# Optimization experiments

Hardware: AMD Instinct MI355X
Metric: run time of the kernel (lower is better)

Reference implementation:

```python
import jax, jax.numpy as jnp
import numpy as np

B, C, N, K = 2, 64, 20000, 16
COUT = 64


def setup_inputs() -> dict:
    key = jax.random.key(0)
    k1, k2, k3, k4, k5 = jax.random.split(key, 5)
    x = jax.random.normal(k1, (B, C, N, 1), dtype=jnp.float32)
    edge_index = jax.random.randint(k2, (2, B, N, K), 0, N)
    pos = jax.random.normal(k3, (B, 3, N, 1), dtype=jnp.float32)
    # BasicConv([2C, COUT]) -> 1x1 Conv2d weight [COUT, 2C] (+bias), then ReLU
    W = jax.random.normal(k4, (COUT, 2 * C), dtype=jnp.float32) * (1.0 / np.sqrt(2 * C))
    b = jax.random.normal(k5, (COUT,), dtype=jnp.float32) * 0.01
    return {"x": x, "edge_index": edge_index, "pos": pos, "W": W, "b": b}


def _gather(t, idx):
    # t: [B, C, N, 1], idx: [B, N, K] -> [B, C, N, K]
    t3 = t[..., 0]  # [B, C, N]
    return jax.vmap(lambda tb, ib: tb[:, ib])(t3, idx)


def reference(x, edge_index, pos, W, b):
    x_i = _gather(x, edge_index[1])           # [B, C, N, K] center
    x_j = _gather(x, edge_index[0])           # [B, C, N, K] neighbor
    feat = jnp.concatenate([x_i, x_j - x_i], axis=1)  # [B, 2C, N, K]
    # 1x1 conv + bias + ReLU
    out = jnp.einsum('oc,bcnk->bonk', W, feat) + b[None, :, None, None]
    out = jax.nn.relu(out)
    # distance-based suppression
    pos_i = _gather(pos, edge_index[1])       # [B, 3, N, K]
    pos_j = _gather(pos, edge_index[0])
    dis = jnp.sqrt(jnp.sum(jnp.square(pos_j - pos_i), axis=1))  # [B, N, K]
    suppression = 2.0 * jax.nn.sigmoid(-dis)[:, None, :, :]     # [B, 1, N, K]
    out = out * suppression
    max_value = jnp.max(out, axis=-1, keepdims=True)             # [B, COUT, N, 1]
    return max_value
```

## Files before the change

### kernel.cpp

```cpp
#include <hip/hip_runtime.h>
#include <math.h>

#define B_    2
#define C_    64
#define N_    20000
#define K_    16
#define COUT_ 64
#define TN1   64
#define NB1   ((N_ + TN1 - 1) / TN1)
#define TN2   16
#define NB2   (N_ / TN2)

typedef unsigned int   u32;
typedef unsigned short u16;

static __device__ __forceinline__ u16 f2bf(float f) {
    union { float f; u32 u; } v; v.f = f;
    u32 r = (v.u + 0x7FFFu + ((v.u >> 16) & 1u)) >> 16;
    return (u16)r;
}
static __device__ __forceinline__ float uasf(u32 u) {
    union { u32 u; float f; } v; v.u = u; return v.f;
}

__global__ __launch_bounds__(256)
void stage1(const float* __restrict__ x, const float* __restrict__ W,
            const float* __restrict__ bias,
            u16* __restrict__ zbuf, u16* __restrict__ ybuf) {
    __shared__ float xt[64][68];
    __shared__ float wc[64][130];

    const int bi   = blockIdx.x;
    const int b    = bi / NB1;
    const int n0   = (bi % NB1) * TN1;
    const int t    = threadIdx.x;
    const int lane = t & 63;
    const int w    = t >> 6;

    #pragma unroll
    for (int r = 0; r < 16; ++r) {
        int flat = r * 256 + t;
        int o = flat >> 6, c = flat & 63;
        float w1 = W[o * 128 + c];
        float w2 = W[o * 128 + 64 + c];
        wc[c][2 * o]     = w1 - w2;
        wc[c][2 * o + 1] = w2;
    }
    const float* xb = x + (size_t)b * C_ * N_;
    #pragma unroll
    for (int r = 0; r < 4; ++r) {
        int flat = r * 256 + t;
        int c = flat >> 4, ng = (flat & 15) * 4;
        int n = n0 + ng;
        float4 v;
        if (n + 3 < N_) {
            v = *(const float4*)&xb[c * N_ + n];
        } else {
            v.x = (n     < N_) ? xb[c * N_ + n    ] : 0.0f;
            v.y = (n + 1 < N_) ? xb[c * N_ + n + 1] : 0.0f;
            v.z = (n + 2 < N_) ? xb[c * N_ + n + 2] : 0.0f;
            v.w = (n + 3 < N_) ? xb[c * N_ + n + 3] : 0.0f;
        }
        *(float4*)&xt[c][ng] = v;
    }
    const float bo = bias[lane];
    __syncthreads();

    const int nb = w * 16;
    float4 z0 = {bo,bo,bo,bo}, z1 = z0, z2 = z0, z3 = z0;
    float4 y0 = {0,0,0,0},     y1 = y0, y2 = y0, y3 = y0;

#define FMA4(ZR, YR, XV) \
    ZR.x = fmaf(wv.x, XV.x, ZR.x);  YR.x = fmaf(wv.y, XV.x, YR.x); \
    ZR.y = fmaf(wv.x, XV.y, ZR.y);  YR.y = fmaf(wv.y, XV.y, YR.y); \
    ZR.z = fmaf(wv.x, XV.z, ZR.z);  YR.z = fmaf(wv.y, XV.z, YR.z); \
    ZR.w = fmaf(wv.x, XV.w, ZR.w);  YR.w = fmaf(wv.y, XV.w, YR.w);

    #pragma unroll 2
    for (int c = 0; c < 64; ++c) {
        float2 wv = *(const float2*)&wc[c][2 * lane];
        float4 xa = *(const float4*)&xt[c][nb];
        float4 xv1 = *(const float4*)&xt[c][nb + 4];
        float4 xv2 = *(const float4*)&xt[c][nb + 8];
        float4 xv3 = *(const float4*)&xt[c][nb + 12];
        FMA4(z0, y0, xa)
        FMA4(z1, y1, xv1)
        FMA4(z2, y2, xv2)
        FMA4(z3, y3, xv3)
    }
#undef FMA4

    {
        const size_t rowb = (size_t)b * N_;
        auto st = [&](int i, float zv, float yv) {
            int n = n0 + nb + i;
            if (n < N_) {
                size_t off = (rowb + n) * 64 + lane;
                zbuf[off] = f2bf(zv);
                ybuf[off] = f2bf(yv);
            }
        };
        st(0,  z0.x, y0.x); st(1,  z0.y, y0.y); st(2,  z0.z, y0.z); st(3,  z0.w, y0.w);
        st(4,  z1.x, y1.x); st(5,  z1.y, y1.y); st(6,  z1.z, y1.z); st(7,  z1.w, y1.w);
        st(8,  z2.x, y2.x); st(9,  z2.y, y2.y); st(10, z2.z, y2.z); st(11, z2.w, y2.w);
        st(12, z3.x, y3.x); st(13, z3.y, y3.y); st(14, z3.z, y3.z); st(15, z3.w, y3.w);
    }
}

__global__ __launch_bounds__(256)
void stage2(const int* __restrict__ ei, const float* __restrict__ pos,
            const u16* __restrict__ zbuf, const u16* __restrict__ ybuf,
            float* __restrict__ out) {
    __shared__ uint2 esl[TN2][17];
    __shared__ float tile[TN2][66];

    const int bi   = blockIdx.x;
    const int b    = bi / NB2;
    const int n0   = (bi % NB2) * TN2;
    const int t    = threadIdx.x;
    const int nl   = t >> 4;
    const int kh   = (t >> 3) & 1;
    const int cq   = t & 7;

    {
        const int    idx = n0 * K_ + t;
        const int*   e0  = ei + (size_t)b * N_ * K_;
        const int*   e1  = ei + ((size_t)B_ + b) * N_ * K_;
        const float* pb  = pos + (size_t)b * 3 * N_;
        int i0 = e0[idx], i1 = e1[idx];
        float dx = pb[i0]          - pb[i1];
        float dy = pb[N_ + i0]     - pb[N_ + i1];
        float dz = pb[2 * N_ + i0] - pb[2 * N_ + i1];
        float dis = sqrtf(dx * dx + dy * dy + dz * dz);
        float s = 2.0f / (1.0f + __expf(dis));
        esl[t >> 4][t & 15] = make_uint2((u32)i0 | ((u32)i1 << 16),
                                         __float_as_uint(s));
    }
    __syncthreads();

    const u16* zb = zbuf + (size_t)b * N_ * 64;
    const u16* yb = ybuf + (size_t)b * N_ * 64;

    float4 ma = {0,0,0,0}, mb = {0,0,0,0};

#define COMB(ZW, YW, MLO, MHI) { \
    float zl = uasf((ZW) << 16), zh = uasf((ZW) & 0xFFFF0000u); \
    float yl = uasf((YW) << 16), yh = uasf((YW) & 0xFFFF0000u); \
    MLO = fmaxf(MLO, fmaxf(zl + yl, 0.0f) * s); \
    MHI = fmaxf(MHI, fmaxf(zh + yh, 0.0f) * s); }

    #pragma unroll
    for (int i = 0; i < 8; ++i) {
        int   k = 2 * i + kh;
        uint2 e = esl[nl][k];
        int   i0 = (int)(e.x & 0xFFFFu);
        int   i1 = (int)(e.x >> 16);
        float s  = uasf(e.y);
        uint4 z4 = *((const uint4*)(zb + ((size_t)i1 << 6)) + cq);
        uint4 y4 = *((const uint4*)(yb + ((size_t)i0 << 6)) + cq);
        COMB(z4.x, y4.x, ma.x, ma.y)
        COMB(z4.y, y4.y, ma.z, ma.w)
        COMB(z4.z, y4.z, mb.x, mb.y)
        COMB(z4.w, y4.w, mb.z, mb.w)
    }
#undef COMB

    ma.x = fmaxf(ma.x, __shfl_xor(ma.x, 8));
    ma.y = fmaxf(ma.y, __shfl_xor(ma.y, 8));
    ma.z = fmaxf(ma.z, __shfl_xor(ma.z, 8));
    ma.w = fmaxf(ma.w, __shfl_xor(ma.w, 8));
    mb.x = fmaxf(mb.x, __shfl_xor(mb.x, 8));
    mb.y = fmaxf(mb.y, __shfl_xor(mb.y, 8));
    mb.z = fmaxf(mb.z, __shfl_xor(mb.z, 8));
    mb.w = fmaxf(mb.w, __shfl_xor(mb.w, 8));

    if (kh == 0) {
        int cb = cq * 8;
        *(float2*)&tile[nl][cb]     = make_float2(ma.x, ma.y);
        *(float2*)&tile[nl][cb + 2] = make_float2(ma.z, ma.w);
        *(float2*)&tile[nl][cb + 4] = make_float2(mb.x, mb.y);
        *(float2*)&tile[nl][cb + 6] = make_float2(mb.z, mb.w);
    }
    __syncthreads();

    #pragma unroll
    for (int r = 0; r < 4; ++r) {
        int flat = r * 256 + t;
        int o = flat >> 4, n2 = flat & 15;
        __builtin_nontemporal_store(tile[n2][o],
            &out[((size_t)b * COUT_ + o) * N_ + n0 + n2]);
    }
}

extern "C" void kernel_launch(void* const* d_in, const int* in_sizes, int n_in,
                              void* d_out, int out_size, void* d_ws, size_t ws_size,
                              hipStream_t stream) {
    const float* x    = (const float*)d_in[0];
    const int*   ei   = (const int*)  d_in[1];
    const float* pos  = (const float*)d_in[2];
    const float* W    = (const float*)d_in[3];
    const float* bias = (const float*)d_in[4];
    float*       out  = (float*)d_out;

    const size_t tabElems = (size_t)B_ * N_ * 64;
    u16* zbuf = (u16*)d_ws;
    u16* ybuf = zbuf + tabElems;

    hipLaunchKernelGGL(stage1, dim3(B_ * NB1), dim3(256), 0, stream,
                       x, W, bias, zbuf, ybuf);
    hipLaunchKernelGGL(stage2, dim3(B_ * NB2), dim3(256), 0, stream,
                       ei, pos, zbuf, ybuf, out);
}
```

Baseline: 107.9 us.

## Split gather tables into channel halves and precompute edge data in separate kernel

Stage1 now writes the z/y bf16 tables split into two 32-channel halves, and stage2 runs one block per channel half, so each block gathers from a half-sized table region that may fit better in cache. Edge indices and distance suppression factors are computed once in a new edgeprep kernel and stored as packed uint2, which removes the redundant per-block pos gathers. Stage2 reads these from global memory and reduces across four k-slices with two shuffle rounds. The trade-off is an extra kernel launch plus a round trip of the edge buffer through memory, and the edge data is now read twice, once per channel half.

```diff
diff --git a/kernel.cpp b/kernel.cpp
--- a/kernel.cpp
+++ b/kernel.cpp
@@ -10,6 +10,7 @@
 #define NB1   ((N_ + TN1 - 1) / TN1)
 #define TN2   16
 #define NB2   (N_ / TN2)
+#define NCH   2
 
 typedef unsigned int   u32;
 typedef unsigned short u16;
@@ -21,6 +22,22 @@
 }
 static __device__ __forceinline__ float uasf(u32 u) {
     union { u32 u; float f; } v; v.u = u; return v.f;
+}
+
+__global__ __launch_bounds__(256)
+void edgeprep(const int* __restrict__ ei, const float* __restrict__ pos,
+              uint2* __restrict__ ebuf) {
+    const int g  = blockIdx.x * 256 + threadIdx.x;
+    const int b  = g / (N_ * K_);
+    const int i0 = ei[g];
+    const int i1 = ei[B_ * N_ * K_ + g];
+    const float* pb = pos + (size_t)b * 3 * N_;
+    float dx = pb[i0]          - pb[i1];
+    float dy = pb[N_ + i0]     - pb[N_ + i1];
+    float dz = pb[2 * N_ + i0] - pb[2 * N_ + i1];
+    float dis = sqrtf(dx * dx + dy * dy + dz * dz);
+    float s = 2.0f / (1.0f + __expf(dis));
+    ebuf[g] = make_uint2((u32)i0 | ((u32)i1 << 16), __float_as_uint(s));
 }
 
 __global__ __launch_bounds__(256)
@@ -91,11 +108,11 @@
 #undef FMA4
 
     {
-        const size_t rowb = (size_t)b * N_;
+        const size_t chb = ((size_t)(lane >> 5) * B_ + b) * N_;
         auto st = [&](int i, float zv, float yv) {
             int n = n0 + nb + i;
             if (n < N_) {
-                size_t off = (rowb + n) * 64 + lane;
+                size_t off = (chb + n) * 32 + (lane & 31);
                 zbuf[off] = f2bf(zv);
                 ybuf[off] = f2bf(yv);
             }
@@ -108,38 +125,24 @@
 }
 
 __global__ __launch_bounds__(256)
-void stage2(const int* __restrict__ ei, const float* __restrict__ pos,
+void stage2(const uint2* __restrict__ ebuf,
             const u16* __restrict__ zbuf, const u16* __restrict__ ybuf,
             float* __restrict__ out) {
-    __shared__ uint2 esl[TN2][17];
-    __shared__ float tile[TN2][66];
-
-    const int bi   = blockIdx.x;
-    const int b    = bi / NB2;
-    const int n0   = (bi % NB2) * TN2;
-    const int t    = threadIdx.x;
-    const int nl   = t >> 4;
-    const int kh   = (t >> 3) & 1;
-    const int cq   = t & 7;
-
-    {
-        const int    idx = n0 * K_ + t;
-        const int*   e0  = ei + (size_t)b * N_ * K_;
-        const int*   e1  = ei + ((size_t)B_ + b) * N_ * K_;
-        const float* pb  = pos + (size_t)b * 3 * N_;
-        int i0 = e0[idx], i1 = e1[idx];
-        float dx = pb[i0]          - pb[i1];
-        float dy = pb[N_ + i0]     - pb[N_ + i1];
-        float dz = pb[2 * N_ + i0] - pb[2 * N_ + i1];
-        float dis = sqrtf(dx * dx + dy * dy + dz * dz);
-        float s = 2.0f / (1.0f + __expf(dis));
-        esl[t >> 4][t & 15] = make_uint2((u32)i0 | ((u32)i1 << 16),
-                                         __float_as_uint(s));
-    }
-    __syncthreads();
-
-    const u16* zb = zbuf + (size_t)b * N_ * 64;
-    const u16* yb = ybuf + (size_t)b * N_ * 64;
+    __shared__ float tile[TN2][34];
+
+    const int bi  = blockIdx.x;
+    const int b   = bi / (NCH * NB2);
+    const int rem = bi % (NCH * NB2);
+    const int ch  = rem / NB2;
+    const int n0  = (rem % NB2) * TN2;
+    const int t   = threadIdx.x;
+    const int nl  = t >> 4;
+    const int ks  = (t >> 2) & 3;
+    const int cq  = t & 3;
+
+    const uint2* eb = ebuf + (size_t)b * N_ * K_ + (size_t)(n0 + nl) * K_ + ks;
+    const u16*   zb = zbuf + ((size_t)ch * B_ + b) * N_ * 32;
+    const u16*   yb = ybuf + ((size_t)ch * B_ + b) * N_ * 32;
 
     float4 ma = {0,0,0,0}, mb = {0,0,0,0};
 
@@ -150,14 +153,13 @@
     MHI = fmaxf(MHI, fmaxf(zh + yh, 0.0f) * s); }
 
     #pragma unroll
-    for (int i = 0; i < 8; ++i) {
-        int   k = 2 * i + kh;
-        uint2 e = esl[nl][k];
+    for (int i = 0; i < 4; ++i) {
+        uint2 e = eb[4 * i];
         int   i0 = (int)(e.x & 0xFFFFu);
         int   i1 = (int)(e.x >> 16);
         float s  = uasf(e.y);
-        uint4 z4 = *((const uint4*)(zb + ((size_t)i1 << 6)) + cq);
-        uint4 y4 = *((const uint4*)(yb + ((size_t)i0 << 6)) + cq);
+        uint4 z4 = *((const uint4*)(zb + ((size_t)i1 << 5)) + cq);
+        uint4 y4 = *((const uint4*)(yb + ((size_t)i0 << 5)) + cq);
         COMB(z4.x, y4.x, ma.x, ma.y)
         COMB(z4.y, y4.y, ma.z, ma.w)
         COMB(z4.z, y4.z, mb.x, mb.y)
@@ -165,6 +167,14 @@
     }
 #undef COMB
 
+    ma.x = fmaxf(ma.x, __shfl_xor(ma.x, 4));
+    ma.y = fmaxf(ma.y, __shfl_xor(ma.y, 4));
+    ma.z = fmaxf(ma.z, __shfl_xor(ma.z, 4));
+    ma.w = fmaxf(ma.w, __shfl_xor(ma.w, 4));
+    mb.x = fmaxf(mb.x, __shfl_xor(mb.x, 4));
+    mb.y = fmaxf(mb.y, __shfl_xor(mb.y, 4));
+    mb.z = fmaxf(mb.z, __shfl_xor(mb.z, 4));
+    mb.w = fmaxf(mb.w, __shfl_xor(mb.w, 4));
     ma.x = fmaxf(ma.x, __shfl_xor(ma.x, 8));
     ma.y = fmaxf(ma.y, __shfl_xor(ma.y, 8));
     ma.z = fmaxf(ma.z, __shfl_xor(ma.z, 8));
@@ -174,7 +184,7 @@
     mb.z = fmaxf(mb.z, __shfl_xor(mb.z, 8));
     mb.w = fmaxf(mb.w, __shfl_xor(mb.w, 8));
 
-    if (kh == 0) {
+    if (ks == 0) {
         int cb = cq * 8;
         *(float2*)&tile[nl][cb]     = make_float2(ma.x, ma.y);
         *(float2*)&tile[nl][cb + 2] = make_float2(ma.z, ma.w);
@@ -184,11 +194,11 @@
     __syncthreads();
 
     #pragma unroll
-    for (int r = 0; r < 4; ++r) {
+    for (int r = 0; r < 2; ++r) {
         int flat = r * 256 + t;
         int o = flat >> 4, n2 = flat & 15;
         __builtin_nontemporal_store(tile[n2][o],
-            &out[((size_t)b * COUT_ + o) * N_ + n0 + n2]);
+            &out[((size_t)b * COUT_ + ch * 32 + o) * N_ + n0 + n2]);
     }
 }
 
@@ -202,12 +212,15 @@
     const float* bias = (const float*)d_in[4];
     float*       out  = (float*)d_out;
 
-    const size_t tabElems = (size_t)B_ * N_ * 64;
-    u16* zbuf = (u16*)d_ws;
-    u16* ybuf = zbuf + tabElems;
-
+    const size_t tabElems = (size_t)NCH * B_ * N_ * 32;
+    u16*   zbuf = (u16*)d_ws;
+    u16*   ybuf = zbuf + tabElems;
+    uint2* ebuf = (uint2*)(ybuf + tabElems);
+
+    hipLaunchKernelGGL(edgeprep, dim3((B_ * N_ * K_) / 256), dim3(256), 0, stream,
+                       ei, pos, ebuf);
     hipLaunchKernelGGL(stage1, dim3(B_ * NB1), dim3(256), 0, stream,
                        x, W, bias, zbuf, ybuf);
-    hipLaunchKernelGGL(stage2, dim3(B_ * NB2), dim3(256), 0, stream,
-                       ei, pos, zbuf, ybuf, out);
-}
+    hipLaunchKernelGGL(stage2, dim3(B_ * NCH * NB2), dim3(256), 0, stream,
+                       ebuf, zbuf, ybuf, out);
+}
```

Result: slower. 116.9 us (+8.4%).

## Split gather tables into two channel halves and swizzle stage2 block order

Applied to the files above, without the earlier changes.

Stage1 now writes the bf16 z/y tables as two channel-half planes of 32 channels each instead of one 64-channel row per point. Stage2 launches twice as many blocks, each handling one channel half. A block-index swizzle interleaves batch and half so that concurrently scheduled blocks work on different planes, which is meant to shrink the per-block gather working set and improve cache locality of the random row gathers. In exchange, the edge indices and the distance/suppression computation are recomputed for each half, extra shuffle reductions are added, and the edge-index loads become nontemporal.

```diff
diff --git a/kernel.cpp b/kernel.cpp
--- a/kernel.cpp
+++ b/kernel.cpp
@@ -10,6 +10,7 @@
 #define NB1   ((N_ + TN1 - 1) / TN1)
 #define TN2   16
 #define NB2   (N_ / TN2)
+#define NCH   2
 
 typedef unsigned int   u32;
 typedef unsigned short u16;
@@ -91,11 +92,11 @@
 #undef FMA4
 
     {
-        const size_t rowb = (size_t)b * N_;
+        const size_t chb = ((size_t)(lane >> 5) * B_ + b) * N_;
         auto st = [&](int i, float zv, float yv) {
             int n = n0 + nb + i;
             if (n < N_) {
-                size_t off = (rowb + n) * 64 + lane;
+                size_t off = (chb + n) * 32 + (lane & 31);
                 zbuf[off] = f2bf(zv);
                 ybuf[off] = f2bf(yv);
             }
@@ -112,22 +113,27 @@
             const u16* __restrict__ zbuf, const u16* __restrict__ ybuf,
             float* __restrict__ out) {
     __shared__ uint2 esl[TN2][17];
-    __shared__ float tile[TN2][66];
-
-    const int bi   = blockIdx.x;
-    const int b    = bi / NB2;
-    const int n0   = (bi % NB2) * TN2;
+    __shared__ float tile[TN2][34];
+
+    const int bid  = blockIdx.x;
+    const int x8   = bid & 7;
+    const int p    = x8 & 3;
+    const int b    = p >> 1;
+    const int ch   = p & 1;
+    const int tl   = (bid >> 3) * 2 + (x8 >> 2);
+    const int n0   = tl * TN2;
     const int t    = threadIdx.x;
     const int nl   = t >> 4;
-    const int kh   = (t >> 3) & 1;
-    const int cq   = t & 7;
+    const int ks   = (t >> 2) & 3;
+    const int cq   = t & 3;
 
     {
         const int    idx = n0 * K_ + t;
         const int*   e0  = ei + (size_t)b * N_ * K_;
         const int*   e1  = ei + ((size_t)B_ + b) * N_ * K_;
         const float* pb  = pos + (size_t)b * 3 * N_;
-        int i0 = e0[idx], i1 = e1[idx];
+        int i0 = __builtin_nontemporal_load(&e0[idx]);
+        int i1 = __builtin_nontemporal_load(&e1[idx]);
         float dx = pb[i0]          - pb[i1];
         float dy = pb[N_ + i0]     - pb[N_ + i1];
         float dz = pb[2 * N_ + i0] - pb[2 * N_ + i1];
@@ -138,8 +144,8 @@
     }
     __syncthreads();
 
-    const u16* zb = zbuf + (size_t)b * N_ * 64;
-    const u16* yb = ybuf + (size_t)b * N_ * 64;
+    const u16* zb = zbuf + ((size_t)ch * B_ + b) * N_ * 32;
+    const u16* yb = ybuf + ((size_t)ch * B_ + b) * N_ * 32;
 
     float4 ma = {0,0,0,0}, mb = {0,0,0,0};
 
@@ -150,14 +156,13 @@
     MHI = fmaxf(MHI, fmaxf(zh + yh, 0.0f) * s); }
 
     #pragma unroll
-    for (int i = 0; i < 8; ++i) {
-        int   k = 2 * i + kh;
-        uint2 e = esl[nl][k];
+    for (int i = 0; i < 4; ++i) {
+        uint2 e = esl[nl][4 * i + ks];
         int   i0 = (int)(e.x & 0xFFFFu);
         int   i1 = (int)(e.x >> 16);
         float s  = uasf(e.y);
-        uint4 z4 = *((const uint4*)(zb + ((size_t)i1 << 6)) + cq);
-        uint4 y4 = *((const uint4*)(yb + ((size_t)i0 << 6)) + cq);
+        uint4 z4 = *((const uint4*)(zb + ((size_t)i1 << 5)) + cq);
+        uint4 y4 = *((const uint4*)(yb + ((size_t)i0 << 5)) + cq);
         COMB(z4.x, y4.x, ma.x, ma.y)
         COMB(z4.y, y4.y, ma.z, ma.w)
         COMB(z4.z, y4.z, mb.x, mb.y)
@@ -165,6 +170,14 @@
     }
 #undef COMB
 
+    ma.x = fmaxf(ma.x, __shfl_xor(ma.x, 4));
+    ma.y = fmaxf(ma.y, __shfl_xor(ma.y, 4));
+    ma.z = fmaxf(ma.z, __shfl_xor(ma.z, 4));
+    ma.w = fmaxf(ma.w, __shfl_xor(ma.w, 4));
+    mb.x = fmaxf(mb.x, __shfl_xor(mb.x, 4));
+    mb.y = fmaxf(mb.y, __shfl_xor(mb.y, 4));
+    mb.z = fmaxf(mb.z, __shfl_xor(mb.z, 4));
+    mb.w = fmaxf(mb.w, __shfl_xor(mb.w, 4));
     ma.x = fmaxf(ma.x, __shfl_xor(ma.x, 8));
     ma.y = fmaxf(ma.y, __shfl_xor(ma.y, 8));
     ma.z = fmaxf(ma.z, __shfl_xor(ma.z, 8));
@@ -174,7 +187,7 @@
     mb.z = fmaxf(mb.z, __shfl_xor(mb.z, 8));
     mb.w = fmaxf(mb.w, __shfl_xor(mb.w, 8));
 
-    if (kh == 0) {
+    if (ks == 0) {
         int cb = cq * 8;
         *(float2*)&tile[nl][cb]     = make_float2(ma.x, ma.y);
         *(float2*)&tile[nl][cb + 2] = make_float2(ma.z, ma.w);
@@ -184,11 +197,11 @@
     __syncthreads();
 
     #pragma unroll
-    for (int r = 0; r < 4; ++r) {
+    for (int r = 0; r < 2; ++r) {
         int flat = r * 256 + t;
         int o = flat >> 4, n2 = flat & 15;
         __builtin_nontemporal_store(tile[n2][o],
-            &out[((size_t)b * COUT_ + o) * N_ + n0 + n2]);
+            &out[((size_t)b * COUT_ + ch * 32 + o) * N_ + n0 + n2]);
     }
 }
 
@@ -202,12 +215,12 @@
     const float* bias = (const float*)d_in[4];
     float*       out  = (float*)d_out;
 
-    const size_t tabElems = (size_t)B_ * N_ * 64;
+    const size_t tabElems = (size_t)NCH * B_ * N_ * 32;
     u16* zbuf = (u16*)d_ws;
     u16* ybuf = zbuf + tabElems;
 
     hipLaunchKernelGGL(stage1, dim3(B_ * NB1), dim3(256), 0, stream,
                        x, W, bias, zbuf, ybuf);
-    hipLaunchKernelGGL(stage2, dim3(B_ * NB2), dim3(256), 0, stream,
+    hipLaunchKernelGGL(stage2, dim3(B_ * NCH * NB2), dim3(256), 0, stream,
                        ei, pos, zbuf, ybuf, out);
 }
```

Measured after the change: 127.9 us. 18.6% more time.

## Give each stage2 thread a full neighbor loop and double nodes per block

Applied to the files above, without the earlier changes.

The gather-max kernel now assigns one node per 8-thread group, and each thread loops over all 16 neighbors. This replaces the previous split of neighbors across two thread halves followed by a cross-lane shuffle reduction. The tile size grows to 32 nodes per block, and edge-index and distance setup now processes two edges per thread with vectorized int2 loads. The goal is more independent gathers in flight per thread and less reduction overhead, at the cost of half as many blocks and longer per-thread dependency chains. The shared tile row stride changed to 65 while float2 stores remain, so those LDS writes can be misaligned on odd rows.

```diff
diff --git a/kernel.cpp b/kernel.cpp
--- a/kernel.cpp
+++ b/kernel.cpp
@@ -8,7 +8,7 @@
 #define COUT_ 64
 #define TN1   64
 #define NB1   ((N_ + TN1 - 1) / TN1)
-#define TN2   16
+#define TN2   32
 #define NB2   (N_ / TN2)
 
 typedef unsigned int   u32;
@@ -112,34 +112,43 @@
             const u16* __restrict__ zbuf, const u16* __restrict__ ybuf,
             float* __restrict__ out) {
     __shared__ uint2 esl[TN2][17];
-    __shared__ float tile[TN2][66];
-
-    const int bi   = blockIdx.x;
-    const int b    = bi / NB2;
-    const int n0   = (bi % NB2) * TN2;
-    const int t    = threadIdx.x;
-    const int nl   = t >> 4;
-    const int kh   = (t >> 3) & 1;
-    const int cq   = t & 7;
+    __shared__ float tile[TN2][65];
+
+    const int bi  = blockIdx.x;
+    const int b   = bi / NB2;
+    const int n0  = (bi % NB2) * TN2;
+    const int t   = threadIdx.x;
+    const int nl  = t >> 3;
+    const int cq  = t & 7;
 
     {
-        const int    idx = n0 * K_ + t;
+        const int    e2  = 2 * t;
+        const int    idx = n0 * K_ + e2;
         const int*   e0  = ei + (size_t)b * N_ * K_;
         const int*   e1  = ei + ((size_t)B_ + b) * N_ * K_;
         const float* pb  = pos + (size_t)b * 3 * N_;
-        int i0 = e0[idx], i1 = e1[idx];
-        float dx = pb[i0]          - pb[i1];
-        float dy = pb[N_ + i0]     - pb[N_ + i1];
-        float dz = pb[2 * N_ + i0] - pb[2 * N_ + i1];
-        float dis = sqrtf(dx * dx + dy * dy + dz * dz);
-        float s = 2.0f / (1.0f + __expf(dis));
-        esl[t >> 4][t & 15] = make_uint2((u32)i0 | ((u32)i1 << 16),
-                                         __float_as_uint(s));
+        int2 i0p = *(const int2*)&e0[idx];
+        int2 i1p = *(const int2*)&e1[idx];
+        float dx0 = pb[i0p.x]          - pb[i1p.x];
+        float dy0 = pb[N_ + i0p.x]     - pb[N_ + i1p.x];
+        float dz0 = pb[2 * N_ + i0p.x] - pb[2 * N_ + i1p.x];
+        float dx1 = pb[i0p.y]          - pb[i1p.y];
+        float dy1 = pb[N_ + i0p.y]     - pb[N_ + i1p.y];
+        float dz1 = pb[2 * N_ + i0p.y] - pb[2 * N_ + i1p.y];
+        float d0 = sqrtf(dx0 * dx0 + dy0 * dy0 + dz0 * dz0);
+        float d1 = sqrtf(dx1 * dx1 + dy1 * dy1 + dz1 * dz1);
+        float s0 = 2.0f / (1.0f + __expf(d0));
+        float s1 = 2.0f / (1.0f + __expf(d1));
+        const int na = e2 >> 4, ka = e2 & 15;
+        esl[na][ka]     = make_uint2((u32)i0p.x | ((u32)i1p.x << 16),
+                                     __float_as_uint(s0));
+        esl[na][ka + 1] = make_uint2((u32)i0p.y | ((u32)i1p.y << 16),
+                                     __float_as_uint(s1));
     }
     __syncthreads();
 
-    const u16* zb = zbuf + (size_t)b * N_ * 64;
-    const u16* yb = ybuf + (size_t)b * N_ * 64;
+    const uint4* zb = (const uint4*)(zbuf + (size_t)b * N_ * 64) + cq;
+    const uint4* yb = (const uint4*)(ybuf + (size_t)b * N_ * 64) + cq;
 
     float4 ma = {0,0,0,0}, mb = {0,0,0,0};
 
@@ -150,14 +159,13 @@
     MHI = fmaxf(MHI, fmaxf(zh + yh, 0.0f) * s); }
 
     #pragma unroll
-    for (int i = 0; i < 8; ++i) {
-        int   k = 2 * i + kh;
+    for (int k = 0; k < 16; ++k) {
         uint2 e = esl[nl][k];
         int   i0 = (int)(e.x & 0xFFFFu);
         int   i1 = (int)(e.x >> 16);
         float s  = uasf(e.y);
-        uint4 z4 = *((const uint4*)(zb + ((size_t)i1 << 6)) + cq);
-        uint4 y4 = *((const uint4*)(yb + ((size_t)i0 << 6)) + cq);
+        uint4 z4 = zb[(size_t)i1 << 3];
+        uint4 y4 = yb[(size_t)i0 << 3];
         COMB(z4.x, y4.x, ma.x, ma.y)
         COMB(z4.y, y4.y, ma.z, ma.w)
         COMB(z4.z, y4.z, mb.x, mb.y)
@@ -165,16 +173,7 @@
     }
 #undef COMB
 
-    ma.x = fmaxf(ma.x, __shfl_xor(ma.x, 8));
-    ma.y = fmaxf(ma.y, __shfl_xor(ma.y, 8));
-    ma.z = fmaxf(ma.z, __shfl_xor(ma.z, 8));
-    ma.w = fmaxf(ma.w, __shfl_xor(ma.w, 8));
-    mb.x = fmaxf(mb.x, __shfl_xor(mb.x, 8));
-    mb.y = fmaxf(mb.y, __shfl_xor(mb.y, 8));
-    mb.z = fmaxf(mb.z, __shfl_xor(mb.z, 8));
-    mb.w = fmaxf(mb.w, __shfl_xor(mb.w, 8));
-
-    if (kh == 0) {
+    {
         int cb = cq * 8;
         *(float2*)&tile[nl][cb]     = make_float2(ma.x, ma.y);
         *(float2*)&tile[nl][cb + 2] = make_float2(ma.z, ma.w);
@@ -184,9 +183,9 @@
     __syncthreads();
 
     #pragma unroll
-    for (int r = 0; r < 4; ++r) {
+    for (int r = 0; r < 8; ++r) {
         int flat = r * 256 + t;
-        int o = flat >> 4, n2 = flat & 15;
+        int o = flat >> 5, n2 = flat & 31;
         __builtin_nontemporal_store(tile[n2][o],
             &out[((size_t)b * COUT_ + o) * N_ + n0 + n2]);
     }
```

Result: no change. 109.3 us (+1.4%).
